# Kernel tuning notes

Hardware: AMD Instinct MI355X
Metric: run time of the kernel (lower is better)

Reference implementation:

```python
import jax, jax.numpy as jnp
import numpy as np

N_A, N_B = 50000, 50000
E = 500000
IN, H, OUT, NGRAPHS = 128, 128, 10, 64
# (src_type, dst_type) per edge type, matching metadata[1]
EDGE_TYPES = [(0, 0), (0, 1), (1, 0), (1, 1)]
NUM_LAYERS = 2
NEG_SLOPE = 0.2  # GATConv leaky_relu slope


def setup_inputs() -> dict:
    key = jax.random.key(0)
    ks = jax.random.split(key, 16)
    ei = [jax.random.randint(ks[2 + e], (2, E), 0, 50000).astype(jnp.int32) for e in range(4)]
    return {
        "x_A": jax.random.normal(ks[0], (N_A, IN), jnp.float32),
        "x_B": jax.random.normal(ks[1], (N_B, IN), jnp.float32),
        "ei0": ei[0], "ei1": ei[1], "ei2": ei[2], "ei3": ei[3],
        "batch_A": jnp.sort(jax.random.randint(ks[6], (N_A,), 0, NGRAPHS)).astype(jnp.int32),
        "batch_B": jnp.sort(jax.random.randint(ks[7], (N_B,), 0, NGRAPHS)).astype(jnp.int32),
        "batch_size": NGRAPHS,
        "w_src": jax.random.normal(ks[8], (NUM_LAYERS, 4, IN, H), jnp.float32) * 0.05,
        "w_dst": jax.random.normal(ks[9], (NUM_LAYERS, 4, IN, H), jnp.float32) * 0.05,
        "att_src": jax.random.normal(ks[10], (NUM_LAYERS, 4, H), jnp.float32) * 0.05,
        "att_dst": jax.random.normal(ks[11], (NUM_LAYERS, 4, H), jnp.float32) * 0.05,
        "conv_bias": jax.random.normal(ks[12], (NUM_LAYERS, 4, H), jnp.float32) * 0.05,
        "wc": jax.random.normal(ks[13], (2 * H, OUT), jnp.float32) * 0.05,
        "bc": jax.random.normal(ks[14], (OUT,), jnp.float32) * 0.05,
    }


def gat_conv(x_src, x_dst, edge_index, ws, wd, a_s, a_d, b, num_dst):
    # PyG GATConv, heads=1, add_self_loops=False, aggr='mean'
    h_src = x_src @ ws            # [Ns, H]
    h_dst = x_dst @ wd            # [Nd, H]
    s_src = h_src @ a_s           # [Ns]
    s_dst = h_dst @ a_d           # [Nd]
    src, dst = edge_index[0], edge_index[1]
    score = jax.nn.leaky_relu(s_src[src] + s_dst[dst], NEG_SLOPE)  # [E]
    # segment softmax over destination nodes
    smax = jax.ops.segment_max(score, dst, num_segments=num_dst)
    ex = jnp.exp(score - smax[dst])
    denom = jax.ops.segment_sum(ex, dst, num_segments=num_dst)
    alpha = ex / denom[dst]
    msg = alpha[:, None] * h_src[src]                               # [E, H]
    summed = jax.ops.segment_sum(msg, dst, num_segments=num_dst)
    cnt = jax.ops.segment_sum(jnp.ones_like(alpha), dst, num_segments=num_dst)
    return summed / jnp.maximum(cnt, 1.0)[:, None] + b


def mean_pool(x, batch, batch_size):
    s = jax.ops.segment_sum(x, batch, num_segments=batch_size)
    c = jax.ops.segment_sum(jnp.ones((x.shape[0],), x.dtype), batch, num_segments=batch_size)
    return s / jnp.maximum(c, 1.0)[:, None]


def reference(x_A, x_B, ei0, ei1, ei2, ei3, batch_A, batch_B, batch_size,
              w_src, w_dst, att_src, att_dst, conv_bias, wc, bc):
    xs = [x_A, x_B]
    eis = [ei0, ei1, ei2, ei3]
    for L in range(NUM_LAYERS):
        outs = {0: [], 1: []}
        for e, (st, dt) in enumerate(EDGE_TYPES):
            o = gat_conv(xs[st], xs[dt], eis[e], w_src[L, e], w_dst[L, e],
                         att_src[L, e], att_dst[L, e], conv_bias[L, e], xs[dt].shape[0])
            outs[dt].append(o)
        # HeteroConv inter_aggr='mean' across edge types, then relu (dropout is identity in eval)
        xs = [jax.nn.relu(jnp.mean(jnp.stack(outs[t], 0), 0)) for t in (0, 1)]
    pooled = [mean_pool(xs[0], batch_A, batch_size), mean_pool(xs[1], batch_B, batch_size)]
    graph_emb = jnp.concatenate(pooled, axis=1)  # [B, 2H]
    return graph_emb @ wc + bc
```

## Files before the change

kernel.cpp:

```cpp
#include <hip/hip_runtime.h>
#include <hip/hip_bf16.h>

#define NN 50000
#define EE 500000
#define GG 64
#define NSL 50
#define SPAN 1000
#define NCH 125
#define EPG (EE / NCH)
#define NCNT (4 * NSL * NCH)
#define SCB ((NCNT + 255) / 256)

typedef __attribute__((ext_vector_type(8))) short bf16x8;
typedef __attribute__((ext_vector_type(4))) float f32x4;

__device__ __forceinline__ float wred_sum(float v) {
#pragma unroll
  for (int s = 32; s; s >>= 1) v += __shfl_xor(v, s, 64);
  return v;
}
__device__ __forceinline__ float gred_sum(float v) {
  v += __shfl_xor(v, 1, 64);
  v += __shfl_xor(v, 2, 64);
  v += __shfl_xor(v, 4, 64);
  v += __shfl_xor(v, 8, 64);
  return v;
}

__device__ __forceinline__ short f2bf(float x) {
  __hip_bfloat16 b = __float2bfloat16(x);
  return *reinterpret_cast<short*>(&b);
}
__device__ __forceinline__ float bf2f(unsigned short s) {
  __hip_bfloat16 b = *reinterpret_cast<__hip_bfloat16*>(&s);
  return __bfloat162float(b);
}

__global__ __launch_bounds__(256) void v_kernel(const float* wdst, const float* adst, float* v) {
  int wv = (blockIdx.x * 256 + threadIdx.x) >> 6;
  int lane = threadIdx.x & 63;
  int le = wv >> 7, k = wv & 127;
  const float* W = wdst + (size_t)le * 16384 + k * 128;
  const float* a = adst + le * 128;
  float p = W[lane] * a[lane] + W[64 + lane] * a[64 + lane];
  p = wred_sum(p);
  if (lane == 0) v[le * 128 + k] = p;
}

__global__ __launch_bounds__(256) void wcvt_kernel(const float* wsrc, short* whiT, short* wloT) {
  int idx = blockIdx.x * 256 + threadIdx.x;
  int le = idx >> 14, rem = idx & 16383;
  int c = rem >> 7, k = rem & 127;
  float v = wsrc[(size_t)le * 16384 + k * 128 + c];
  short hi = f2bf(v);
  whiT[idx] = hi;
  wloT[idx] = f2bf(v - bf2f((unsigned short)hi));
}


__global__ __launch_bounds__(256) void pcount_kernel(const int* e0, const int* e1, const int* e2,
                                                     const int* e3, int* counts) {
  int t = blockIdx.y, ch = blockIdx.x;
  const int* ei = (t == 0 ? e0 : t == 1 ? e1 : t == 2 ? e2 : e3);
  const int* dst = ei + EE;
  __shared__ int cnt[NSL];
  for (int i = threadIdx.x; i < NSL; i += 256) cnt[i] = 0;
  __syncthreads();
  int i0 = ch * EPG;
  for (int i = i0 + threadIdx.x; i < i0 + EPG; i += 256) atomicAdd(&cnt[dst[i] / SPAN], 1);
  __syncthreads();
  for (int sl = threadIdx.x; sl < NSL; sl += 256) counts[(t * NSL + sl) * NCH + ch] = cnt[sl];
}

__global__ __launch_bounds__(256) void scan1_kernel(const int* counts, int* bsums) {
  int tid = threadIdx.x, lane = tid & 63, wid = tid >> 6;
  int idx = blockIdx.x * 256 + tid;
  int v = (idx < NCNT) ? counts[idx] : 0;
#pragma unroll
  for (int s = 32; s; s >>= 1) v += __shfl_xor(v, s, 64);
  __shared__ int ws[4];
  if (lane == 0) ws[wid] = v;
  __syncthreads();
  if (tid == 0) bsums[blockIdx.x] = ws[0] + ws[1] + ws[2] + ws[3];
}

__global__ void scan2_kernel(int* bsums) {
  __shared__ int s[SCB];
  int tid = threadIdx.x;
  if (tid < SCB) s[tid] = bsums[tid];
  __syncthreads();
  if (tid == 0) {
    int run = 0;
    for (int i = 0; i < SCB; i++) { int x = s[i]; s[i] = run; run += x; }
  }
  __syncthreads();
  if (tid < SCB) bsums[tid] = s[tid];
}

__global__ __launch_bounds__(256) void scan3_kernel(int* counts, const int* bsums, int* sliceptr) {
  int tid = threadIdx.x, lane = tid & 63, wid = tid >> 6;
  int idx = blockIdx.x * 256 + tid;
  int v = (idx < NCNT) ? counts[idx] : 0;
  int orig = v;
#pragma unroll
  for (int s = 1; s < 64; s <<= 1) { int u = __shfl_up(v, s, 64); if (lane >= s) v += u; }
  __shared__ int ws[4];
  if (lane == 63) ws[wid] = v;
  __syncthreads();
  int woff = (wid > 0 ? ws[0] : 0) + (wid > 1 ? ws[1] : 0) + (wid > 2 ? ws[2] : 0);
  int excl = bsums[blockIdx.x] + woff + v - orig;
  if (idx < NCNT) {
    counts[idx] = excl;
    if (idx % NCH == 0) {
      int g = idx / NCH;
      sliceptr[(g / NSL) * (NSL + 1) + (g % NSL)] = excl;
    }
  }
  if (blockIdx.x == 0 && tid < 4) sliceptr[tid * (NSL + 1) + NSL] = (tid + 1) * EE;
}

__global__ __launch_bounds__(256) void ppart_kernel(const int* e0, const int* e1, const int* e2,
                                                    const int* e3, const int* counts, int2* pairs) {
  int t = blockIdx.y, ch = blockIdx.x;
  const int* ei = (t == 0 ? e0 : t == 1 ? e1 : t == 2 ? e2 : e3);
  const int* srcr = ei;
  const int* dstr = ei + EE;
  __shared__ int cur[NSL];
  for (int i = threadIdx.x; i < NSL; i += 256) cur[i] = counts[(t * NSL + i) * NCH + ch];
  __syncthreads();
  int i0 = ch * EPG;
  for (int i = i0 + threadIdx.x; i < i0 + EPG; i += 256) {
    int d = dstr[i], s = srcr[i];
    int pos = atomicAdd(&cur[d / SPAN], 1);
    pairs[pos] = make_int2(s, d);
  }
}

__global__ __launch_bounds__(256) void pbuild_kernel(const int2* pairs, const int* sliceptr,
                                                     int* rowptr, int* col) {
  int t = blockIdx.y, sl = blockIdx.x;
  int n0 = sl * SPAN;
  int e0 = sliceptr[t * (NSL + 1) + sl], e1 = sliceptr[t * (NSL + 1) + sl + 1];
  int tid = threadIdx.x, lane = tid & 63, wid = tid >> 6;
  __shared__ int cnt[SPAN];
  __shared__ int wsum[4];
  for (int i = tid; i < SPAN; i += 256) cnt[i] = 0;
  __syncthreads();
  for (int e = e0 + tid; e < e1; e += 256) atomicAdd(&cnt[pairs[e].y - n0], 1);
  __syncthreads();
  int s0 = 0, s1 = 0, s2 = 0, s3 = 0, tot = 0;
  if (tid < SPAN / 4) {
    s0 = cnt[tid * 4]; s1 = cnt[tid * 4 + 1]; s2 = cnt[tid * 4 + 2]; s3 = cnt[tid * 4 + 3];
    tot = s0 + s1 + s2 + s3;
  }
  int v = tot;
#pragma unroll
  for (int sft = 1; sft < 64; sft <<= 1) { int u = __shfl_up(v, sft, 64); if (lane >= sft) v += u; }
  if (lane == 63) wsum[wid] = v;
  __syncthreads();
  int woffv = (wid > 0 ? wsum[0] : 0) + (wid > 1 ? wsum[1] : 0) + (wid > 2 ? wsum[2] : 0);
  int excl = v + woffv - tot;
  __syncthreads();
  if (tid < SPAN / 4) {
    cnt[tid * 4] = excl;
    cnt[tid * 4 + 1] = excl + s0;
    cnt[tid * 4 + 2] = excl + s0 + s1;
    cnt[tid * 4 + 3] = excl + s0 + s1 + s2;
  }
  __syncthreads();
  int base = e0 - t * EE;
  for (int n = tid; n < SPAN; n += 256) rowptr[(size_t)t * (NN + 1) + n0 + n] = base + cnt[n];
  if (sl == NSL - 1 && tid == 0) rowptr[(size_t)t * (NN + 1) + NN] = EE;
  __syncthreads();
  int* ct = col + (size_t)t * EE;
  for (int e = e0 + tid; e < e1; e += 256) {
    int2 p = pairs[e];
    int pos = base + atomicAdd(&cnt[p.y - n0], 1);
    ct[pos] = p.x;
  }
}

__global__ void gbound_kernel(const int* batchA, const int* batchB, int* gbA, int* gbB) {
  int t = threadIdx.x;
  if (t >= 130) return;
  int which = t / 65, g = t % 65;
  const int* b = which ? batchB : batchA;
  int* gb = which ? gbB : gbA;
  int lo = 0, hi = NN;
  while (lo < hi) { int mid = (lo + hi) >> 1; if (b[mid] < g) lo = mid + 1; else hi = mid; }
  gb[g] = lo;
}

#define SWZ(row, kb) ((((row) << 6) + (kb)) ^ (((row) & 7) << 4))
#define HSTRIDE 136

__device__ __forceinline__ void cvt8(const float4 a, const float4 b, bf16x8& hv, bf16x8& lv) {
  short h;
  h = f2bf(a.x); hv[0] = h; lv[0] = f2bf(a.x - bf2f((unsigned short)h));
  h = f2bf(a.y); hv[1] = h; lv[1] = f2bf(a.y - bf2f((unsigned short)h));
  h = f2bf(a.z); hv[2] = h; lv[2] = f2bf(a.z - bf2f((unsigned short)h));
  h = f2bf(a.w); hv[3] = h; lv[3] = f2bf(a.w - bf2f((unsigned short)h));
  h = f2bf(b.x); hv[4] = h; lv[4] = f2bf(b.x - bf2f((unsigned short)h));
  h = f2bf(b.y); hv[5] = h; lv[5] = f2bf(b.y - bf2f((unsigned short)h));
  h = f2bf(b.z); hv[6] = h; lv[6] = f2bf(b.z - bf2f((unsigned short)h));
  h = f2bf(b.w); hv[7] = h; lv[7] = f2bf(b.w - bf2f((unsigned short)h));
}

__global__ __launch_bounds__(256) void gemm_hs_kernel(
    const float* X0_, const float* X1_,
    const short* whiT, const short* wloT,
    const float* attsrc,
    unsigned short* h4, float* s4) {
  int e = blockIdx.z;
  const float* X = (e < 2) ? X0_ : X1_;
  const short* Wh = whiT + (size_t)e * 16384;
  const short* Wl = wloT + (size_t)e * 16384;
  const float* att = attsrc + e * 128;
  unsigned short* h = h4 + (size_t)e * NN * 128;
  float* s_ = s4 + (size_t)e * NN;

  __shared__ short smem[16384];
  short* Ah = smem;
  short* Al = smem + 4096;
  short* Bh = smem + 8192;
  short* Bl = smem + 12288;

  int tid = threadIdx.x;
  int l = tid & 63, w = tid >> 6;
  int arow = l & 15;
  int kb = (l >> 4) << 4;
  int row0 = blockIdx.x * 128;

  f32x4 acc[2][8];
#pragma unroll
  for (int i = 0; i < 2; i++)
#pragma unroll
    for (int j = 0; j < 8; j++) acc[i][j] = (f32x4){0.f, 0.f, 0.f, 0.f};

  float attr[8];
#pragma unroll
  for (int j = 0; j < 8; j++) attr[j] = att[j * 16 + arow];

  int sr = tid >> 1, half = tid & 1;
  int xrow = row0 + sr; xrow = xrow < NN ? xrow : NN - 1;
  const float* xbase = X + (size_t)xrow * 128 + half * 16;
  const short* whbase = Wh + sr * 128 + half * 16;
  const short* wlbase = Wl + sr * 128 + half * 16;
  int soff0 = SWZ(sr, half * 32);
  int soff1 = SWZ(sr, half * 32 + 16);

  float4 f0 = *(const float4*)(xbase);
  float4 f1 = *(const float4*)(xbase + 4);
  float4 f2 = *(const float4*)(xbase + 8);
  float4 f3 = *(const float4*)(xbase + 12);
  bf16x8 wh0 = *(const bf16x8*)(whbase);
  bf16x8 wh1 = *(const bf16x8*)(whbase + 8);
  bf16x8 wl0 = *(const bf16x8*)(wlbase);
  bf16x8 wl1 = *(const bf16x8*)(wlbase + 8);

  for (int kt = 0; kt < 128; kt += 32) {
    bf16x8 hv0, lv0, hv1, lv1;
    cvt8(f0, f1, hv0, lv0);
    cvt8(f2, f3, hv1, lv1);
    *(bf16x8*)((char*)Ah + soff0) = hv0;
    *(bf16x8*)((char*)Ah + soff1) = hv1;
    *(bf16x8*)((char*)Al + soff0) = lv0;
    *(bf16x8*)((char*)Al + soff1) = lv1;
    *(bf16x8*)((char*)Bh + soff0) = wh0;
    *(bf16x8*)((char*)Bh + soff1) = wh1;
    *(bf16x8*)((char*)Bl + soff0) = wl0;
    *(bf16x8*)((char*)Bl + soff1) = wl1;
    __syncthreads();

    if (kt < 96) {
      f0 = *(const float4*)(xbase + kt + 32);
      f1 = *(const float4*)(xbase + kt + 36);
      f2 = *(const float4*)(xbase + kt + 40);
      f3 = *(const float4*)(xbase + kt + 44);
      wh0 = *(const bf16x8*)(whbase + kt + 32);
      wh1 = *(const bf16x8*)(whbase + kt + 40);
      wl0 = *(const bf16x8*)(wlbase + kt + 32);
      wl1 = *(const bf16x8*)(wlbase + kt + 40);
    }

    bf16x8 ah[2], al[2];
#pragma unroll
    for (int i = 0; i < 2; i++) {
      int row = w * 32 + i * 16 + arow;
      ah[i] = *(bf16x8*)((char*)Ah + SWZ(row, kb));
      al[i] = *(bf16x8*)((char*)Al + SWZ(row, kb));
    }
#pragma unroll
    for (int j = 0; j < 8; j++) {
      int colr = j * 16 + arow;
      bf16x8 bh = *(bf16x8*)((char*)Bh + SWZ(colr, kb));
      bf16x8 bl = *(bf16x8*)((char*)Bl + SWZ(colr, kb));
#pragma unroll
      for (int i = 0; i < 2; i++) {
        acc[i][j] = __builtin_amdgcn_mfma_f32_16x16x32_bf16(ah[i], bh, acc[i][j], 0, 0, 0);
        acc[i][j] = __builtin_amdgcn_mfma_f32_16x16x32_bf16(ah[i], bl, acc[i][j], 0, 0, 0);
        acc[i][j] = __builtin_amdgcn_mfma_f32_16x16x32_bf16(al[i], bh, acc[i][j], 0, 0, 0);
      }
    }
    __syncthreads();
  }

#pragma unroll
  for (int p = 0; p < 2; p++) {
    if ((w >> 1) == p) {
#pragma unroll
      for (int i = 0; i < 2; i++) {
#pragma unroll
        for (int r = 0; r < 4; r++) {
          int lrow = (w & 1) * 32 + i * 16 + ((l >> 4) << 2) + r;
          int row = row0 + p * 64 + lrow;
          float pp = 0.f;
#pragma unroll
          for (int j = 0; j < 8; j++) pp += acc[i][j][r] * attr[j];
          pp += __shfl_xor(pp, 1, 64);
          pp += __shfl_xor(pp, 2, 64);
          pp += __shfl_xor(pp, 4, 64);
          pp += __shfl_xor(pp, 8, 64);
          if (row < NN && arow == 0) s_[row] = pp;
#pragma unroll
          for (int j = 0; j < 8; j++) smem[lrow * HSTRIDE + j * 16 + arow] = f2bf(acc[i][j][r]);
        }
      }
    }
    __syncthreads();
#pragma unroll
    for (int it = 0; it < 4; it++) {
      int idx = it * 256 + tid;
      int lrow = idx >> 4, c8 = idx & 15;
      int row = row0 + p * 64 + lrow;
      if (row < NN)
        *(bf16x8*)(h + (size_t)row * 128 + c8 * 8) = *(const bf16x8*)(smem + lrow * HSTRIDE + c8 * 8);
    }
    __syncthreads();
  }
}

#define ACC8(a, uv, wv)                             \
  do {                                              \
    a[0] += wv * __uint_as_float(uv.x << 16);       \
    a[1] += wv * __uint_as_float(uv.x & 0xffff0000u); \
    a[2] += wv * __uint_as_float(uv.y << 16);       \
    a[3] += wv * __uint_as_float(uv.y & 0xffff0000u); \
    a[4] += wv * __uint_as_float(uv.z << 16);       \
    a[5] += wv * __uint_as_float(uv.z & 0xffff0000u); \
    a[6] += wv * __uint_as_float(uv.w << 16);       \
    a[7] += wv * __uint_as_float(uv.w & 0xffff0000u); \
  } while (0)

__global__ __launch_bounds__(256) void agg_kernel(
    const float* xdst,
    const int* rpA, const int* colA, const unsigned short* hA_, const float* sA_, const float* vA, const float* bA,
    const int* rpB, const int* colB, const unsigned short* hB_, const float* sB_, const float* vB, const float* bB,
    float* Y) {
  int lane = threadIdx.x & 63;
  int q = lane & 15;
  int gb = lane & 48;
  int t = (lane >> 4) & 1;
  int node = blockIdx.x * 8 + (threadIdx.x >> 5);
  if (node >= NN) return;
  int d0 = q * 8;
  const float* xr = xdst + (size_t)node * 128 + d0;
  float4 xv0 = *(const float4*)(xr);
  float4 xv1 = *(const float4*)(xr + 4);

  const int* rp = t ? rpB : rpA;
  const int* cl = t ? colB : colA;
  const unsigned short* h = t ? hB_ : hA_;
  const float* ss = t ? sB_ : sA_;
  const float* v = t ? vB : vA;
  const float* b = t ? bB : bA;
  const uint4* hq = (const uint4*)h + q;

  float4 v0 = *(const float4*)(v + d0);
  float4 v1 = *(const float4*)(v + d0 + 4);
  float part = xv0.x * v0.x + xv0.y * v0.y + xv0.z * v0.z + xv0.w * v0.w +
               xv1.x * v1.x + xv1.y * v1.y + xv1.z * v1.z + xv1.w * v1.w;
  float sd = gred_sum(part);

  int start = rp[node], end = rp[node + 1];
  int deg = end - start;

  float dsum = 0.f;
  float a[8] = {0.f, 0.f, 0.f, 0.f, 0.f, 0.f, 0.f, 0.f};

  for (int base2 = start; base2 < end; base2 += 16) {
    int i = base2 + q;
    int src = 0;
    float ex = 0.f;
    if (i < end) {
      src = cl[i];
      float s = ss[src] + sd;
      s = (s >= 0.f) ? s : 0.2f * s;
      ex = __expf(s);
    }
    dsum += ex;
    int cT = min(16, end - base2);
    int j = 0;
    for (; j + 3 < cT; j += 4) {
      int sj0 = __shfl(src, gb + j, 64);     float e0 = __shfl(ex, gb + j, 64);
      int sj1 = __shfl(src, gb + j + 1, 64); float e1 = __shfl(ex, gb + j + 1, 64);
      int sj2 = __shfl(src, gb + j + 2, 64); float e2 = __shfl(ex, gb + j + 2, 64);
      int sj3 = __shfl(src, gb + j + 3, 64); float e3 = __shfl(ex, gb + j + 3, 64);
      uint4 uv0 = hq[(size_t)sj0 * 16];
      uint4 uv1 = hq[(size_t)sj1 * 16];
      uint4 uv2 = hq[(size_t)sj2 * 16];
      uint4 uv3 = hq[(size_t)sj3 * 16];
      ACC8(a, uv0, e0);
      ACC8(a, uv1, e1);
      ACC8(a, uv2, e2);
      ACC8(a, uv3, e3);
    }
    for (; j < cT; j++) {
      int sj = __shfl(src, gb + j, 64);
      float ej = __shfl(ex, gb + j, 64);
      uint4 uv = hq[(size_t)sj * 16];
      ACC8(a, uv, ej);
    }
  }

  float denom = gred_sum(dsum);
  float inv = (deg > 0) ? 0.5f / (denom * (float)deg) : 0.f;
  float outv[8];
#pragma unroll
  for (int k2 = 0; k2 < 8; k2++) outv[k2] = a[k2] * inv + 0.5f * b[d0 + k2];

#pragma unroll
  for (int k2 = 0; k2 < 8; k2++) outv[k2] += __shfl_xor(outv[k2], 16, 64);

  if (!(lane & 16)) {
    float4 o0 = make_float4(fmaxf(outv[0], 0.f), fmaxf(outv[1], 0.f), fmaxf(outv[2], 0.f), fmaxf(outv[3], 0.f));
    float4 o1 = make_float4(fmaxf(outv[4], 0.f), fmaxf(outv[5], 0.f), fmaxf(outv[6], 0.f), fmaxf(outv[7], 0.f));
    *(float4*)(Y + (size_t)node * 128 + d0) = o0;
    *(float4*)(Y + (size_t)node * 128 + d0 + 4) = o1;
  }
}

__global__ __launch_bounds__(128) void pool_part_kernel(const float* XA_, const float* XB_,
                                                        const int* gbA, const int* gbB,
                                                        float* pooled) {
  int t = blockIdx.y, g = blockIdx.x, c = blockIdx.z;
  const float* X = t ? XB_ : XA_;
  const int* gb = t ? gbB : gbA;
  int n0 = gb[g], n1 = gb[g + 1];
  int dim = threadIdx.x;
  float s = 0.f;
  for (int node = n0 + c; node < n1; node += 8) s += X[(size_t)node * 128 + dim];
  atomicAdd(&pooled[g * 256 + t * 128 + dim], s);
}

__global__ void final_kernel(const float* pooled, const int* gbA, const int* gbB,
                             const float* wc, const float* bc, float* out) {
  int tid = blockIdx.x * blockDim.x + threadIdx.x;
  if (tid >= GG * 10) return;
  int g = tid / 10, o = tid % 10;
  float invA = 1.f / fmaxf((float)(gbA[g + 1] - gbA[g]), 1.f);
  float invB = 1.f / fmaxf((float)(gbB[g + 1] - gbB[g]), 1.f);
  float acc = bc[o];
  for (int k = 0; k < 256; k++)
    acc += pooled[g * 256 + k] * (k < 128 ? invA : invB) * wc[k * 10 + o];
  out[g * 10 + o] = acc;
}

extern "C" void kernel_launch(void* const* d_in, const int* in_sizes, int n_in,
                              void* d_out, int out_size, void* d_ws, size_t ws_size,
                              hipStream_t stream) {
  const float* xA = (const float*)d_in[0];
  const float* xB = (const float*)d_in[1];
  const int* ei0 = (const int*)d_in[2];
  const int* ei1 = (const int*)d_in[3];
  const int* ei2 = (const int*)d_in[4];
  const int* ei3 = (const int*)d_in[5];
  const int* batchA = (const int*)d_in[6];
  const int* batchB = (const int*)d_in[7];
  const float* wsrc = (const float*)d_in[9];
  const float* wdst = (const float*)d_in[10];
  const float* attsrc = (const float*)d_in[11];
  const float* attdst = (const float*)d_in[12];
  const float* cbias = (const float*)d_in[13];
  const float* wc = (const float*)d_in[14];
  const float* bc = (const float*)d_in[15];
  float* out = (float*)d_out;

  char* ws = (char*)d_ws;
  size_t off = 0;
  auto alloc = [&](size_t bytes) { size_t o = off; off += (bytes + 255) & ~(size_t)255; return o; };
  size_t o_rowptr = alloc((size_t)4 * (NN + 1) * 4);
  size_t o_col    = alloc((size_t)4 * EE * 4);
  size_t o_cnts   = alloc((size_t)NCNT * 4);
  size_t o_bsums  = alloc((size_t)SCB * 4);
  size_t o_slptr  = alloc((size_t)4 * (NSL + 1) * 4);
  size_t o_v      = alloc((size_t)8 * 128 * 4);
  size_t o_whiT   = alloc((size_t)8 * 16384 * 2);
  size_t o_wloT   = alloc((size_t)8 * 16384 * 2);
  size_t o_h4     = alloc((size_t)4 * NN * 128 * 2);
  size_t o_s4     = alloc((size_t)4 * NN * 4);
  size_t o_Xa1    = alloc((size_t)NN * 128 * 4);
  size_t o_Xb1    = alloc((size_t)NN * 128 * 4);
  size_t o_Xa2    = alloc((size_t)NN * 128 * 4);
  size_t o_Xb2    = alloc((size_t)NN * 128 * 4);
  size_t o_pooled = alloc((size_t)GG * 256 * 4);
  size_t o_gb     = alloc((size_t)2 * (GG + 1) * 4);

  int* rowptr = (int*)(ws + o_rowptr);
  int* col = (int*)(ws + o_col);
  int* counts = (int*)(ws + o_cnts);
  int* bsums = (int*)(ws + o_bsums);
  int* sliceptr = (int*)(ws + o_slptr);
  float* vv = (float*)(ws + o_v);
  short* whiT = (short*)(ws + o_whiT);
  short* wloT = (short*)(ws + o_wloT);
  unsigned short* h4 = (unsigned short*)(ws + o_h4);
  float* s4 = (float*)(ws + o_s4);
  int2* pairs = (int2*)(ws + o_h4);
  float* Xa1 = (float*)(ws + o_Xa1);
  float* Xb1 = (float*)(ws + o_Xb1);
  float* Xa2 = (float*)(ws + o_Xa2);
  float* Xb2 = (float*)(ws + o_Xb2);
  float* pooled = (float*)(ws + o_pooled);
  int* gbA = (int*)(ws + o_gb);
  int* gbB = gbA + (GG + 1);

  hipMemsetAsync(pooled, 0, (size_t)GG * 256 * 4, stream);

  v_kernel<<<256, 256, 0, stream>>>(wdst, attdst, vv);
  wcvt_kernel<<<512, 256, 0, stream>>>(wsrc, whiT, wloT);
  gbound_kernel<<<1, 192, 0, stream>>>(batchA, batchB, gbA, gbB);
  pcount_kernel<<<dim3(NCH, 4), 256, 0, stream>>>(ei0, ei1, ei2, ei3, counts);
  scan1_kernel<<<SCB, 256, 0, stream>>>(counts, bsums);
  scan2_kernel<<<1, 128, 0, stream>>>(bsums);
  scan3_kernel<<<SCB, 256, 0, stream>>>(counts, bsums, sliceptr);
  ppart_kernel<<<dim3(NCH, 4), 256, 0, stream>>>(ei0, ei1, ei2, ei3, counts, pairs);
  pbuild_kernel<<<dim3(NSL, 4), 256, 0, stream>>>(pairs, sliceptr, rowptr, col);

  int gemm_gx = (NN + 127) / 128;
  int agg_gx = (NN + 7) / 8;

  for (int L = 0; L < 2; L++) {
    const float* X0 = (L == 0) ? xA : Xa1;
    const float* X1 = (L == 0) ? xB : Xb1;
    float* Y0 = (L == 0) ? Xa1 : Xa2;
    float* Y1 = (L == 0) ? Xb1 : Xb2;

    gemm_hs_kernel<<<dim3(gemm_gx, 1, 4), 256, 0, stream>>>(
        X0, X1, whiT + (size_t)L * 4 * 16384, wloT + (size_t)L * 4 * 16384,
        attsrc + L * 4 * 128, h4, s4);

    agg_kernel<<<agg_gx, 256, 0, stream>>>(
        X0,
        rowptr + (size_t)0 * (NN + 1), col + (size_t)0 * EE, h4 + (size_t)0 * NN * 128, s4 + (size_t)0 * NN,
        vv + (L * 4 + 0) * 128, cbias + (L * 4 + 0) * 128,
        rowptr + (size_t)2 * (NN + 1), col + (size_t)2 * EE, h4 + (size_t)2 * NN * 128, s4 + (size_t)2 * NN,
        vv + (L * 4 + 2) * 128, cbias + (L * 4 + 2) * 128,
        Y0);

    agg_kernel<<<agg_gx, 256, 0, stream>>>(
        X1,
        rowptr + (size_t)1 * (NN + 1), col + (size_t)1 * EE, h4 + (size_t)1 * NN * 128, s4 + (size_t)1 * NN,
        vv + (L * 4 + 1) * 128, cbias + (L * 4 + 1) * 128,
        rowptr + (size_t)3 * (NN + 1), col + (size_t)3 * EE, h4 + (size_t)3 * NN * 128, s4 + (size_t)3 * NN,
        vv + (L * 4 + 3) * 128, cbias + (L * 4 + 3) * 128,
        Y1);
  }

  pool_part_kernel<<<dim3(GG, 2, 8), 128, 0, stream>>>(Xa2, Xb2, gbA, gbB, pooled);
  final_kernel<<<3, 256, 0, stream>>>(pooled, gbA, gbB, wc, bc, out);
}
```

Measured before the change: 374.9 us.

## Store intermediate layer activations in bf16 and drop split-precision MFMA for them

Layer outputs Xa/Xb are now written as bf16 instead of fp32, halving their write traffic and the read traffic in the second-layer GEMM, the aggregation kernel and pooling. Because the layer-1 input is already bf16, the GEMM skips the hi/lo split on the activation side, removing one of the three MFMAs per tile and the Al shared-memory traffic. This loses precision relative to the fp32 reference (activations rounded to bf16 before layer 2 and pooling), which may affect accuracy tolerance.

```diff
diff --git a/kernel.cpp b/kernel.cpp
--- a/kernel.cpp
+++ b/kernel.cpp
@@ -206,13 +206,14 @@
   h = f2bf(b.w); hv[7] = h; lv[7] = f2bf(b.w - bf2f((unsigned short)h));
 }
 
+template <bool XBF>
 __global__ __launch_bounds__(256) void gemm_hs_kernel(
-    const float* X0_, const float* X1_,
+    const void* X0_, const void* X1_,
     const short* whiT, const short* wloT,
     const float* attsrc,
     unsigned short* h4, float* s4) {
   int e = blockIdx.z;
-  const float* X = (e < 2) ? X0_ : X1_;
+  const void* X = (e < 2) ? X0_ : X1_;
   const short* Wh = whiT + (size_t)e * 16384;
   const short* Wl = wloT + (size_t)e * 16384;
   const float* att = attsrc + e * 128;
@@ -243,29 +244,44 @@
 
   int sr = tid >> 1, half = tid & 1;
   int xrow = row0 + sr; xrow = xrow < NN ? xrow : NN - 1;
-  const float* xbase = X + (size_t)xrow * 128 + half * 16;
+  const float* xbaseF = nullptr;
+  const short* xbaseH = nullptr;
+  if constexpr (XBF) xbaseH = (const short*)X + (size_t)xrow * 128 + half * 16;
+  else               xbaseF = (const float*)X + (size_t)xrow * 128 + half * 16;
   const short* whbase = Wh + sr * 128 + half * 16;
   const short* wlbase = Wl + sr * 128 + half * 16;
   int soff0 = SWZ(sr, half * 32);
   int soff1 = SWZ(sr, half * 32 + 16);
 
-  float4 f0 = *(const float4*)(xbase);
-  float4 f1 = *(const float4*)(xbase + 4);
-  float4 f2 = *(const float4*)(xbase + 8);
-  float4 f3 = *(const float4*)(xbase + 12);
+  float4 f0, f1, f2, f3;
+  bf16x8 xh0, xh1;
+  if constexpr (XBF) {
+    xh0 = *(const bf16x8*)(xbaseH);
+    xh1 = *(const bf16x8*)(xbaseH + 8);
+  } else {
+    f0 = *(const float4*)(xbaseF);
+    f1 = *(const float4*)(xbaseF + 4);
+    f2 = *(const float4*)(xbaseF + 8);
+    f3 = *(const float4*)(xbaseF + 12);
+  }
   bf16x8 wh0 = *(const bf16x8*)(whbase);
   bf16x8 wh1 = *(const bf16x8*)(whbase + 8);
   bf16x8 wl0 = *(const bf16x8*)(wlbase);
   bf16x8 wl1 = *(const bf16x8*)(wlbase + 8);
 
   for (int kt = 0; kt < 128; kt += 32) {
-    bf16x8 hv0, lv0, hv1, lv1;
-    cvt8(f0, f1, hv0, lv0);
-    cvt8(f2, f3, hv1, lv1);
-    *(bf16x8*)((char*)Ah + soff0) = hv0;
-    *(bf16x8*)((char*)Ah + soff1) = hv1;
-    *(bf16x8*)((char*)Al + soff0) = lv0;
-    *(bf16x8*)((char*)Al + soff1) = lv1;
+    if constexpr (XBF) {
+      *(bf16x8*)((char*)Ah + soff0) = xh0;
+      *(bf16x8*)((char*)Ah + soff1) = xh1;
+    } else {
+      bf16x8 hv0, lv0, hv1, lv1;
+      cvt8(f0, f1, hv0, lv0);
+      cvt8(f2, f3, hv1, lv1);
+      *(bf16x8*)((char*)Ah + soff0) = hv0;
+      *(bf16x8*)((char*)Ah + soff1) = hv1;
+      *(bf16x8*)((char*)Al + soff0) = lv0;
+      *(bf16x8*)((char*)Al + soff1) = lv1;
+    }
     *(bf16x8*)((char*)Bh + soff0) = wh0;
     *(bf16x8*)((char*)Bh + soff1) = wh1;
     *(bf16x8*)((char*)Bl + soff0) = wl0;
@@ -273,10 +289,15 @@
     __syncthreads();
 
     if (kt < 96) {
-      f0 = *(const float4*)(xbase + kt + 32);
-      f1 = *(const float4*)(xbase + kt + 36);
-      f2 = *(const float4*)(xbase + kt + 40);
-      f3 = *(const float4*)(xbase + kt + 44);
+      if constexpr (XBF) {
+        xh0 = *(const bf16x8*)(xbaseH + kt + 32);
+        xh1 = *(const bf16x8*)(xbaseH + kt + 40);
+      } else {
+        f0 = *(const float4*)(xbaseF + kt + 32);
+        f1 = *(const float4*)(xbaseF + kt + 36);
+        f2 = *(const float4*)(xbaseF + kt + 40);
+        f3 = *(const float4*)(xbaseF + kt + 44);
+      }
       wh0 = *(const bf16x8*)(whbase + kt + 32);
       wh1 = *(const bf16x8*)(whbase + kt + 40);
       wl0 = *(const bf16x8*)(wlbase + kt + 32);
@@ -288,7 +309,7 @@
     for (int i = 0; i < 2; i++) {
       int row = w * 32 + i * 16 + arow;
       ah[i] = *(bf16x8*)((char*)Ah + SWZ(row, kb));
-      al[i] = *(bf16x8*)((char*)Al + SWZ(row, kb));
+      if constexpr (!XBF) al[i] = *(bf16x8*)((char*)Al + SWZ(row, kb));
     }
 #pragma unroll
     for (int j = 0; j < 8; j++) {
@@ -299,7 +320,8 @@
       for (int i = 0; i < 2; i++) {
         acc[i][j] = __builtin_amdgcn_mfma_f32_16x16x32_bf16(ah[i], bh, acc[i][j], 0, 0, 0);
         acc[i][j] = __builtin_amdgcn_mfma_f32_16x16x32_bf16(ah[i], bl, acc[i][j], 0, 0, 0);
-        acc[i][j] = __builtin_amdgcn_mfma_f32_16x16x32_bf16(al[i], bh, acc[i][j], 0, 0, 0);
+        if constexpr (!XBF)
+          acc[i][j] = __builtin_amdgcn_mfma_f32_16x16x32_bf16(al[i], bh, acc[i][j], 0, 0, 0);
       }
     }
     __syncthreads();
@@ -352,11 +374,12 @@
     a[7] += wv * __uint_as_float(uv.w & 0xffff0000u); \
   } while (0)
 
+template <bool XBF>
 __global__ __launch_bounds__(256) void agg_kernel(
-    const float* xdst,
+    const void* xdst_,
     const int* rpA, const int* colA, const unsigned short* hA_, const float* sA_, const float* vA, const float* bA,
     const int* rpB, const int* colB, const unsigned short* hB_, const float* sB_, const float* vB, const float* bB,
-    float* Y) {
+    unsigned short* Y) {
   int lane = threadIdx.x & 63;
   int q = lane & 15;
   int gb = lane & 48;
@@ -364,9 +387,19 @@
   int node = blockIdx.x * 8 + (threadIdx.x >> 5);
   if (node >= NN) return;
   int d0 = q * 8;
-  const float* xr = xdst + (size_t)node * 128 + d0;
-  float4 xv0 = *(const float4*)(xr);
-  float4 xv1 = *(const float4*)(xr + 4);
+  float4 xv0, xv1;
+  if constexpr (XBF) {
+    const unsigned short* xr = (const unsigned short*)xdst_ + (size_t)node * 128 + d0;
+    uint4 u = *(const uint4*)xr;
+    xv0 = make_float4(__uint_as_float(u.x << 16), __uint_as_float(u.x & 0xffff0000u),
+                      __uint_as_float(u.y << 16), __uint_as_float(u.y & 0xffff0000u));
+    xv1 = make_float4(__uint_as_float(u.z << 16), __uint_as_float(u.z & 0xffff0000u),
+                      __uint_as_float(u.w << 16), __uint_as_float(u.w & 0xffff0000u));
+  } else {
+    const float* xr = (const float*)xdst_ + (size_t)node * 128 + d0;
+    xv0 = *(const float4*)(xr);
+    xv1 = *(const float4*)(xr + 4);
+  }
 
   const int* rp = t ? rpB : rpA;
   const int* cl = t ? colB : colA;
@@ -433,24 +466,29 @@
   for (int k2 = 0; k2 < 8; k2++) outv[k2] += __shfl_xor(outv[k2], 16, 64);
 
   if (!(lane & 16)) {
-    float4 o0 = make_float4(fmaxf(outv[0], 0.f), fmaxf(outv[1], 0.f), fmaxf(outv[2], 0.f), fmaxf(outv[3], 0.f));
-    float4 o1 = make_float4(fmaxf(outv[4], 0.f), fmaxf(outv[5], 0.f), fmaxf(outv[6], 0.f), fmaxf(outv[7], 0.f));
-    *(float4*)(Y + (size_t)node * 128 + d0) = o0;
-    *(float4*)(Y + (size_t)node * 128 + d0 + 4) = o1;
-  }
-}
-
-__global__ __launch_bounds__(128) void pool_part_kernel(const float* XA_, const float* XB_,
-                                                        const int* gbA, const int* gbB,
-                                                        float* pooled) {
+    bf16x8 o;
+#pragma unroll
+    for (int k2 = 0; k2 < 8; k2++) o[k2] = f2bf(fmaxf(outv[k2], 0.f));
+    *(bf16x8*)(Y + (size_t)node * 128 + d0) = o;
+  }
+}
+
+__global__ __launch_bounds__(64) void pool_part_kernel(const unsigned short* XA_, const unsigned short* XB_,
+                                                       const int* gbA, const int* gbB,
+                                                       float* pooled) {
   int t = blockIdx.y, g = blockIdx.x, c = blockIdx.z;
-  const float* X = t ? XB_ : XA_;
+  const unsigned short* X = t ? XB_ : XA_;
   const int* gb = t ? gbB : gbA;
   int n0 = gb[g], n1 = gb[g + 1];
-  int dim = threadIdx.x;
-  float s = 0.f;
-  for (int node = n0 + c; node < n1; node += 8) s += X[(size_t)node * 128 + dim];
-  atomicAdd(&pooled[g * 256 + t * 128 + dim], s);
+  int d = threadIdx.x * 2;
+  float s0 = 0.f, s1 = 0.f;
+  for (int node = n0 + c; node < n1; node += 8) {
+    unsigned int u = *(const unsigned int*)(X + (size_t)node * 128 + d);
+    s0 += __uint_as_float(u << 16);
+    s1 += __uint_as_float(u & 0xffff0000u);
+  }
+  atomicAdd(&pooled[g * 256 + t * 128 + d], s0);
+  atomicAdd(&pooled[g * 256 + t * 128 + d + 1], s1);
 }
 
 __global__ void final_kernel(const float* pooled, const int* gbA, const int* gbB,
@@ -499,10 +537,10 @@
   size_t o_wloT   = alloc((size_t)8 * 16384 * 2);
   size_t o_h4     = alloc((size_t)4 * NN * 128 * 2);
   size_t o_s4     = alloc((size_t)4 * NN * 4);
-  size_t o_Xa1    = alloc((size_t)NN * 128 * 4);
-  size_t o_Xb1    = alloc((size_t)NN * 128 * 4);
-  size_t o_Xa2    = alloc((size_t)NN * 128 * 4);
-  size_t o_Xb2    = alloc((size_t)NN * 128 * 4);
+  size_t o_Xa1    = alloc((size_t)NN * 128 * 2);
+  size_t o_Xb1    = alloc((size_t)NN * 128 * 2);
+  size_t o_Xa2    = alloc((size_t)NN * 128 * 2);
+  size_t o_Xb2    = alloc((size_t)NN * 128 * 2);
   size_t o_pooled = alloc((size_t)GG * 256 * 4);
   size_t o_gb     = alloc((size_t)2 * (GG + 1) * 4);
 
@@ -517,10 +555,10 @@
   unsigned short* h4 = (unsigned short*)(ws + o_h4);
   float* s4 = (float*)(ws + o_s4);
   int2* pairs = (int2*)(ws + o_h4);
-  float* Xa1 = (float*)(ws + o_Xa1);
-  float* Xb1 = (float*)(ws + o_Xb1);
-  float* Xa2 = (float*)(ws + o_Xa2);
-  float* Xb2 = (float*)(ws + o_Xb2);
+  unsigned short* Xa1 = (unsigned short*)(ws + o_Xa1);
+  unsigned short* Xb1 = (unsigned short*)(ws + o_Xb1);
+  unsigned short* Xa2 = (unsigned short*)(ws + o_Xa2);
+  unsigned short* Xb2 = (unsigned short*)(ws + o_Xb2);
   float* pooled = (float*)(ws + o_pooled);
   int* gbA = (int*)(ws + o_gb);
   int* gbB = gbA + (GG + 1);
@@ -541,32 +579,50 @@
   int agg_gx = (NN + 7) / 8;
 
   for (int L = 0; L < 2; L++) {
-    const float* X0 = (L == 0) ? xA : Xa1;
-    const float* X1 = (L == 0) ? xB : Xb1;
-    float* Y0 = (L == 0) ? Xa1 : Xa2;
-    float* Y1 = (L == 0) ? Xb1 : Xb2;
-
-    gemm_hs_kernel<<<dim3(gemm_gx, 1, 4), 256, 0, stream>>>(
-        X0, X1, whiT + (size_t)L * 4 * 16384, wloT + (size_t)L * 4 * 16384,
-        attsrc + L * 4 * 128, h4, s4);
-
-    agg_kernel<<<agg_gx, 256, 0, stream>>>(
-        X0,
-        rowptr + (size_t)0 * (NN + 1), col + (size_t)0 * EE, h4 + (size_t)0 * NN * 128, s4 + (size_t)0 * NN,
-        vv + (L * 4 + 0) * 128, cbias + (L * 4 + 0) * 128,
-        rowptr + (size_t)2 * (NN + 1), col + (size_t)2 * EE, h4 + (size_t)2 * NN * 128, s4 + (size_t)2 * NN,
-        vv + (L * 4 + 2) * 128, cbias + (L * 4 + 2) * 128,
-        Y0);
-
-    agg_kernel<<<agg_gx, 256, 0, stream>>>(
-        X1,
-        rowptr + (size_t)1 * (NN + 1), col + (size_t)1 * EE, h4 + (size_t)1 * NN * 128, s4 + (size_t)1 * NN,
-        vv + (L * 4 + 1) * 128, cbias + (L * 4 + 1) * 128,
-        rowptr + (size_t)3 * (NN + 1), col + (size_t)3 * EE, h4 + (size_t)3 * NN * 128, s4 + (size_t)3 * NN,
-        vv + (L * 4 + 3) * 128, cbias + (L * 4 + 3) * 128,
-        Y1);
-  }
-
-  pool_part_kernel<<<dim3(GG, 2, 8), 128, 0, stream>>>(Xa2, Xb2, gbA, gbB, pooled);
+    if (L == 0)
+      gemm_hs_kernel<false><<<dim3(gemm_gx, 1, 4), 256, 0, stream>>>(
+          xA, xB, whiT, wloT, attsrc, h4, s4);
+    else
+      gemm_hs_kernel<true><<<dim3(gemm_gx, 1, 4), 256, 0, stream>>>(
+          Xa1, Xb1, whiT + (size_t)4 * 16384, wloT + (size_t)4 * 16384,
+          attsrc + 4 * 128, h4, s4);
+
+    unsigned short* Y0 = (L == 0) ? Xa1 : Xa2;
+    unsigned short* Y1 = (L == 0) ? Xb1 : Xb2;
+    const float* vvL = vv + L * 4 * 128;
+    const float* cbL = cbias + L * 4 * 128;
+
+    if (L == 0)
+      agg_kernel<false><<<agg_gx, 256, 0, stream>>>(
+          xA,
+          rowptr + (size_t)0 * (NN + 1), col + (size_t)0 * EE, h4 + (size_t)0 * NN * 128, s4 + (size_t)0 * NN,
+          vvL + 0 * 128, cbL + 0 * 128,
+          rowptr + (size_t)2 * (NN + 1), col + (size_t)2 * EE, h4 + (size_t)2 * NN * 128, s4 + (size_t)2 * NN,
+          vvL + 2 * 128, cbL + 2 * 128, Y0);
+    else
+      agg_kernel<true><<<agg_gx, 256, 0, stream>>>(
+          Xa1,
+          rowptr + (size_t)0 * (NN + 1), col + (size_t)0 * EE, h4 + (size_t)0 * NN * 128, s4 + (size_t)0 * NN,
+          vvL + 0 * 128, cbL + 0 * 128,
+          rowptr + (size_t)2 * (NN + 1), col + (size_t)2 * EE, h4 + (size_t)2 * NN * 128, s4 + (size_t)2 * NN,
+          vvL + 2 * 128, cbL + 2 * 128, Y0);
+
+    if (L == 0)
+      agg_kernel<false><<<agg_gx, 256, 0, stream>>>(
+          xB,
+          rowptr + (size_t)1 * (NN + 1), col + (size_t)1 * EE, h4 + (size_t)1 * NN * 128, s4 + (size_t)1 * NN,
+          vvL + 1 * 128, cbL + 1 * 128,
+          rowptr + (size_t)3 * (NN + 1), col + (size_t)3 * EE, h4 + (size_t)3 * NN * 128, s4 + (size_t)3 * NN,
+          vvL + 3 * 128, cbL + 3 * 128, Y1);
+    else
+      agg_kernel<true><<<agg_gx, 256, 0, stream>>>(
+          Xb1,
+          rowptr + (size_t)1 * (NN + 1), col + (size_t)1 * EE, h4 + (size_t)1 * NN * 128, s4 + (size_t)1 * NN,
+          vvL + 1 * 128, cbL + 1 * 128,
+          rowptr + (size_t)3 * (NN + 1), col + (size_t)3 * EE, h4 + (size_t)3 * NN * 128, s4 + (size_t)3 * NN,
+          vvL + 3 * 128, cbL + 3 * 128, Y1);
+  }
+
+  pool_part_kernel<<<dim3(GG, 2, 8), 64, 0, stream>>>(Xa2, Xb2, gbA, gbB, pooled);
   final_kernel<<<3, 256, 0, stream>>>(pooled, gbA, gbB, wc, bc, out);
 }
```

Measured after the change: 364.9 us (median of 2 runs). -2.7%, faster.
